# Kernel tuning notes

Hardware: AMD Instinct MI355X
Metric: run time of the kernel (lower is better)

## Reference

```python
import jax, jax.numpy as jnp
import numpy as np

B, N, DIN = 32, 4096, 256
K, D, H = 8, 256, 512
ITERS = 3
EPS = 1e-8
LN_EPS = 1e-5
SCALE = D ** -0.5


def _ln(x, g, b):
    m = jnp.mean(x, axis=-1, keepdims=True)
    v = jnp.var(x, axis=-1, keepdims=True)
    return (x - m) * jax.lax.rsqrt(v + LN_EPS) * g + b


def setup_inputs() -> dict:
    key = jax.random.key(0)
    ks = jax.random.split(key, 12)
    lin = lambda k, o, i: jax.random.uniform(k, (o, i), jnp.float32, -1.0, 1.0) * (i ** -0.5)
    return {
        "x": jax.random.normal(ks[0], (B, N, DIN), jnp.float32),
        "noise": jax.random.normal(ks[1], (B, K, D), jnp.float32),
        "nx_g": jnp.ones((DIN,), jnp.float32), "nx_b": jnp.zeros((DIN,), jnp.float32),
        "ns_g": jnp.ones((D,), jnp.float32), "ns_b": jnp.zeros((D,), jnp.float32),
        "mu": jax.random.normal(ks[2], (1, 1, D), jnp.float32) * 0.02,
        "logsigma": jnp.zeros((1, 1, D), jnp.float32),
        "Wq": lin(ks[3], D, D), "Wk": lin(ks[4], D, DIN), "Wv": lin(ks[5], D, DIN),
        "W_ih": lin(ks[6], 3 * D, D), "W_hh": lin(ks[7], 3 * D, D),
        "b_ih": jnp.zeros((3 * D,), jnp.float32), "b_hh": jnp.zeros((3 * D,), jnp.float32),
        "mlp_g": jnp.ones((D,), jnp.float32), "mlp_b": jnp.zeros((D,), jnp.float32),
        "W1": lin(ks[8], H, D), "b1": jnp.zeros((H,), jnp.float32),
        "W2": lin(ks[9], D, H), "b2": jnp.zeros((D,), jnp.float32),
    }


def _gru(u, h, W_ih, W_hh, b_ih, b_hh):
    # PyTorch GRUCell: gates ordered (r, z, n)
    gi = u @ W_ih.T + b_ih   # [BK, 3D]
    gh = h @ W_hh.T + b_hh
    ir, iz, inn = jnp.split(gi, 3, axis=-1)
    hr, hz, hn = jnp.split(gh, 3, axis=-1)
    r = jax.nn.sigmoid(ir + hr)
    z = jax.nn.sigmoid(iz + hz)
    n = jnp.tanh(inn + r * hn)
    return (1.0 - z) * n + z * h


def reference(x, noise, nx_g, nx_b, ns_g, ns_b, mu, logsigma, Wq, Wk, Wv,
              W_ih, W_hh, b_ih, b_hh, mlp_g, mlp_b, W1, b1, W2, b2):
    xn = _ln(x, nx_g, nx_b)                       # [B,N,DIN]
    k = xn @ Wk.T                                 # [B,N,D]
    v = xn @ Wv.T                                 # [B,N,D]
    slots = mu + jnp.exp(logsigma) * noise        # [B,K,D]
    attn = None
    for _ in range(ITERS):
        s = _ln(slots, ns_g, ns_b)
        q = s @ Wq.T                              # [B,K,D]
        logits = jnp.einsum('bkd,bnd->bkn', q, k) * SCALE
        attn = jax.nn.softmax(logits, axis=1) + EPS   # softmax over slots
        attn = attn / jnp.sum(attn, axis=1, keepdims=True)
        updates = jnp.einsum('bkn,bnd->bkd', attn, v)
        h = _gru(updates.reshape(B * K, D), slots.reshape(B * K, D),
                 W_ih, W_hh, b_ih, b_hh).reshape(B, K, D)
        m = _ln(h, mlp_g, mlp_b)
        m = jax.nn.gelu(m @ W1.T + b1, approximate=False) @ W2.T + b2
        slots = h + m
    return slots, attn
```

## Files before the change

### kernel.cpp

```cpp
#include <hip/hip_runtime.h>
#include <hip/hip_bf16.h>
#include <math.h>

#define LN_EPS 1e-5f
#define EPSA 1e-8f
#define SCALE 0.0625f

typedef __attribute__((ext_vector_type(8))) short short8;
typedef __attribute__((ext_vector_type(4))) short short4_t;
typedef __attribute__((ext_vector_type(4))) float f32x4;

__device__ inline unsigned short f2bf(float f) {
    union { float f; unsigned int u; } v; v.f = f;
    unsigned int r = v.u + 0x7fffu + ((v.u >> 16) & 1u);
    return (unsigned short)(r >> 16);
}
__device__ inline float bf2f(unsigned short h) {
    union { unsigned int u; float f; } v; v.u = ((unsigned int)h) << 16;
    return v.f;
}
__device__ inline float sigmoidf_(float x) { return 1.0f / (1.0f + expf(-x)); }

__global__ __launch_bounds__(256) void pack_wb(const float* __restrict__ Wk,
                                               const float* __restrict__ Wv,
                                               __hip_bfloat16* __restrict__ Wcb) {
    int idx = blockIdx.x * 256 + threadIdx.x;
    int n = idx >> 8, k = idx & 255;
    float v = (n < 256) ? Wk[n*256 + k] : Wv[(n-256)*256 + k];
    Wcb[idx] = __float2bfloat16(v);
}

__global__ __launch_bounds__(256) void gemm_kv_fused(const float* __restrict__ x,
                                                     const float* __restrict__ nx_g,
                                                     const float* __restrict__ nx_b,
                                                     const __hip_bfloat16* __restrict__ Wcb,
                                                     __hip_bfloat16* __restrict__ kp,
                                                     __hip_bfloat16* __restrict__ vp) {
    __shared__ short As[64*256];
    __shared__ float gb[512];
    const int t = threadIdx.x;
    const int row0 = blockIdx.x * 64;
    const int r = t >> 2, q = t & 3;

    float4 xr[16];
    const float* xrow = x + (size_t)(row0 + r) * 256 + q*4;
    #pragma unroll
    for (int j = 0; j < 16; ++j) xr[j] = *(const float4*)(xrow + j*16);
    gb[t] = nx_g[t]; gb[t+256] = nx_b[t];

    float s = 0.f, s2 = 0.f;
    #pragma unroll
    for (int j = 0; j < 16; ++j) {
        s  += xr[j].x + xr[j].y + xr[j].z + xr[j].w;
        s2 += xr[j].x*xr[j].x + xr[j].y*xr[j].y + xr[j].z*xr[j].z + xr[j].w*xr[j].w;
    }
    s  += __shfl_xor(s, 1);  s2 += __shfl_xor(s2, 1);
    s  += __shfl_xor(s, 2);  s2 += __shfl_xor(s2, 2);
    float m = s * (1.0f/256.0f);
    float var = s2 * (1.0f/256.0f) - m*m;
    float rstd = rsqrtf(var + LN_EPS);
    __syncthreads();

    #pragma unroll
    for (int j = 0; j < 16; ++j) {
        int c = q*4 + j*16;
        float4 g = *(const float4*)&gb[c];
        float4 bb = *(const float4*)&gb[256 + c];
        short4_t o;
        o[0] = (short)f2bf((xr[j].x - m)*rstd*g.x + bb.x);
        o[1] = (short)f2bf((xr[j].y - m)*rstd*g.y + bb.y);
        o[2] = (short)f2bf((xr[j].z - m)*rstd*g.z + bb.z);
        o[3] = (short)f2bf((xr[j].w - m)*rstd*g.w + bb.w);
        int byte = ((r << 9) + (c << 1)) ^ ((r & 7) << 4);
        *(short4_t*)((char*)As + byte) = o;
    }
    __syncthreads();

    const int l = t & 63, w = t >> 6;
    const int lr = l & 15, lk = l >> 4;
    const int arow = w*16 + lr;
    short8 af[8];
    #pragma unroll
    for (int ks = 0; ks < 8; ++ks) {
        int lin = (arow << 9) + (lk << 4) + (ks << 6);
        af[ks] = *(short8*)((char*)As + (lin ^ ((arow & 7) << 4)));
    }
    for (int c = 0; c < 8; ++c) {
        f32x4 acc[4];
        #pragma unroll
        for (int bf = 0; bf < 4; ++bf) acc[bf] = (f32x4){0.f,0.f,0.f,0.f};
        #pragma unroll
        for (int ks = 0; ks < 8; ++ks) {
            #pragma unroll
            for (int bf = 0; bf < 4; ++bf) {
                const short8 bv = *(const short8*)((const short*)Wcb +
                    ((size_t)(c*64 + bf*16 + lr))*256 + ks*32 + lk*8);
                acc[bf] = __builtin_amdgcn_mfma_f32_16x16x32_bf16(af[ks], bv, acc[bf], 0, 0, 0);
            }
        }
        __hip_bfloat16* dst = (c < 4) ? kp : vp;
        const int cb = c*64 - ((c >= 4) ? 256 : 0);
        #pragma unroll
        for (int bf = 0; bf < 4; ++bf) {
            int col = cb + bf*16 + lr;
            #pragma unroll
            for (int jj = 0; jj < 4; ++jj) {
                int row = row0 + w*16 + lk*4 + jj;
                dst[(size_t)row*256 + col] = __float2bfloat16(acc[bf][jj]);
            }
        }
    }
}

__global__ __launch_bounds__(256) void slots_init(const float* __restrict__ noise,
                                                  const float* __restrict__ mu,
                                                  const float* __restrict__ logsigma,
                                                  float* __restrict__ slots) {
    int i = blockIdx.x * 256 + threadIdx.x;
    int d = i & 255;
    slots[i] = mu[d] + expf(logsigma[d]) * noise[i];
}

__global__ __launch_bounds__(256) void qproj(const float* __restrict__ slots,
                                             const float* __restrict__ ns_g,
                                             const float* __restrict__ ns_b,
                                             const float* __restrict__ Wq,
                                             unsigned short* __restrict__ qb) {
    int row = blockIdx.x, t = threadIdx.x;
    int b = row >> 3, s8 = row & 7;
    __shared__ float sn[256];
    __shared__ float red[8];
    float v = slots[row*256 + t];
    float s = v, s2 = v*v;
    for (int off = 32; off > 0; off >>= 1) {
        s  += __shfl_down(s, off);
        s2 += __shfl_down(s2, off);
    }
    if ((t & 63) == 0) { red[t>>6] = s; red[4 + (t>>6)] = s2; }
    __syncthreads();
    float S  = red[0]+red[1]+red[2]+red[3];
    float S2 = red[4]+red[5]+red[6]+red[7];
    float m = S * (1.0f/256.0f);
    float var = S2 * (1.0f/256.0f) - m*m;
    float rs = rsqrtf(var + LN_EPS);
    sn[t] = (v - m) * rs * ns_g[t] + ns_b[t];
    __syncthreads();
    float acc = 0.0f;
    const float4* wrow = (const float4*)(Wq + t*256);
    #pragma unroll 8
    for (int i = 0; i < 64; ++i) {
        float4 w = wrow[i];
        acc += w.x*sn[4*i] + w.y*sn[4*i+1] + w.z*sn[4*i+2] + w.w*sn[4*i+3];
    }
    unsigned short hh = f2bf(acc);
    unsigned short ll = f2bf(acc - bf2f(hh));
    qb[((size_t)(b*16 + s8))*256 + t]     = hh;
    qb[((size_t)(b*16 + 8 + s8))*256 + t] = ll;
}

__global__ __launch_bounds__(256) void attn_fused(const __hip_bfloat16* __restrict__ kp,
                                                  const __hip_bfloat16* __restrict__ vp,
                                                  const unsigned short* __restrict__ qb,
                                                  float* __restrict__ attn_out,
                                                  float* __restrict__ partial) {
    __shared__ short as_[16*264];
    __shared__ float asf[8*256];
    const int b = blockIdx.x >> 4, c = blockIdx.x & 15;
    const int t = threadIdx.x, l = t & 63, w = t >> 6;
    const int lr = l & 15, lk = l >> 4;
    const int n0 = c * 256;

    short8 qf[8];
    #pragma unroll
    for (int ks = 0; ks < 8; ++ks)
        qf[ks] = *(const short8*)(qb + ((size_t)(b*16 + lr))*256 + ks*32 + lk*8);

    f32x4 acc[4];
    #pragma unroll
    for (int nf = 0; nf < 4; ++nf) acc[nf] = (f32x4){0.f,0.f,0.f,0.f};
    #pragma unroll
    for (int ks = 0; ks < 8; ++ks) {
        #pragma unroll
        for (int nf = 0; nf < 4; ++nf) {
            const short8 a = *(const short8*)((const short*)kp +
                ((size_t)(b*4096 + n0 + w*64 + nf*16 + lr))*256 + ks*32 + lk*8);
            acc[nf] = __builtin_amdgcn_mfma_f32_16x16x32_bf16(a, qf[ks], acc[nf], 0, 0, 0);
        }
    }

    const float renorm = 1.0f / (1.0f + 8.0f*EPSA);
    #pragma unroll
    for (int nf = 0; nf < 4; ++nf) {
        #pragma unroll
        for (int jj = 0; jj < 4; ++jj) {
            float lg = acc[nf][jj];
            lg += __shfl_xor(lg, 8);
            lg *= SCALE;
            float mx = lg;
            mx = fmaxf(mx, __shfl_xor(mx, 1));
            mx = fmaxf(mx, __shfl_xor(mx, 2));
            mx = fmaxf(mx, __shfl_xor(mx, 4));
            float e = expf(lg - mx);
            float ss = e;
            ss += __shfl_xor(ss, 1);
            ss += __shfl_xor(ss, 2);
            ss += __shfl_xor(ss, 4);
            acc[nf][jj] = (e / ss + EPSA) * renorm;
        }
    }

    if (lr < 8) {
        #pragma unroll
        for (int nf = 0; nf < 4; ++nf) {
            int nl = w*64 + nf*16 + lk*4;
            float4 fa = {acc[nf][0], acc[nf][1], acc[nf][2], acc[nf][3]};
            *(float4*)&asf[lr*256 + nl] = fa;
            short4_t ah, al;
            #pragma unroll
            for (int jj = 0; jj < 4; ++jj) {
                unsigned short h = f2bf(acc[nf][jj]);
                ah[jj] = (short)h;
                al[jj] = (short)f2bf(acc[nf][jj] - bf2f(h));
            }
            *(short4_t*)&as_[lr*264 + nl]       = ah;
            *(short4_t*)&as_[(8 + lr)*264 + nl] = al;
        }
    }
    __syncthreads();

    {
        int slot = t >> 5, nn = (t & 31) * 8;
        float4 f0 = *(float4*)&asf[slot*256 + nn];
        float4 f1 = *(float4*)&asf[slot*256 + nn + 4];
        float* dstp = attn_out + ((size_t)(b*8 + slot))*4096 + n0 + nn;
        *(float4*)dstp = f0;
        *(float4*)(dstp + 4) = f1;
    }

    f32x4 pacc[4];
    #pragma unroll
    for (int df = 0; df < 4; ++df) pacc[df] = (f32x4){0.f,0.f,0.f,0.f};
    #pragma unroll
    for (int ks = 0; ks < 8; ++ks) {
        const short8 a = *(const short8*)&as_[lr*264 + ks*32 + lk*8];
        #pragma unroll
        for (int df = 0; df < 4; ++df) {
            short8 bv;
            #pragma unroll
            for (int j = 0; j < 8; ++j)
                bv[j] = ((const short*)vp)[((size_t)(b*4096 + n0 + ks*32 + lk*8 + j))*256
                                           + w*64 + df*16 + lr];
            pacc[df] = __builtin_amdgcn_mfma_f32_16x16x32_bf16(a, bv, pacc[df], 0, 0, 0);
        }
    }
    #pragma unroll
    for (int df = 0; df < 4; ++df) {
        #pragma unroll
        for (int jj = 0; jj < 4; ++jj) {
            float v = pacc[df][jj];
            float vo = __shfl_xor(v, 32);
            if (l < 32) {
                int slot = lk*4 + jj;
                partial[((size_t)((b*16 + c)*8 + slot))*256 + w*64 + df*16 + lr] = v + vo;
            }
        }
    }
}

__global__ __launch_bounds__(256) void gru_mlp(const float* __restrict__ partial,
                                               const float* __restrict__ slots,
                                               const float* __restrict__ W_ih,
                                               const float* __restrict__ W_hh,
                                               const float* __restrict__ b_ih,
                                               const float* __restrict__ b_hh,
                                               const float* __restrict__ mlp_g,
                                               const float* __restrict__ mlp_b,
                                               const float* __restrict__ W1,
                                               const float* __restrict__ b1,
                                               const float* __restrict__ W2,
                                               const float* __restrict__ b2,
                                               float* __restrict__ slots_out,
                                               float* __restrict__ out_slots,
                                               int last) {
    int rrow = blockIdx.x, t = threadIdx.x;
    int b = rrow >> 3, k = rrow & 7;
    __shared__ float u_s[256], h_s[256];
    __shared__ float hn[256], m1[512];
    __shared__ float red[8];
    float u = 0.0f;
    #pragma unroll
    for (int ch = 0; ch < 16; ++ch)
        u += partial[(((size_t)(b*16 + ch)*8 + k)*256) + t];
    u_s[t] = u;
    h_s[t] = slots[rrow*256 + t];
    __syncthreads();

    float gi_r = b_ih[t], gi_z = b_ih[256 + t], gi_n = b_ih[512 + t];
    float gh_r = b_hh[t], gh_z = b_hh[256 + t], gh_n = b_hh[512 + t];
    const float4* wir = (const float4*)(W_ih + (size_t)t*256);
    const float4* wiz = (const float4*)(W_ih + (size_t)(256 + t)*256);
    const float4* win = (const float4*)(W_ih + (size_t)(512 + t)*256);
    const float4* whr = (const float4*)(W_hh + (size_t)t*256);
    const float4* whz = (const float4*)(W_hh + (size_t)(256 + t)*256);
    const float4* whn = (const float4*)(W_hh + (size_t)(512 + t)*256);
    #pragma unroll 4
    for (int i = 0; i < 64; ++i) {
        float u0 = u_s[4*i], u1 = u_s[4*i+1], u2 = u_s[4*i+2], u3 = u_s[4*i+3];
        float h0 = h_s[4*i], h1 = h_s[4*i+1], h2 = h_s[4*i+2], h3 = h_s[4*i+3];
        float4 wv;
        wv = wir[i]; gi_r += wv.x*u0 + wv.y*u1 + wv.z*u2 + wv.w*u3;
        wv = wiz[i]; gi_z += wv.x*u0 + wv.y*u1 + wv.z*u2 + wv.w*u3;
        wv = win[i]; gi_n += wv.x*u0 + wv.y*u1 + wv.z*u2 + wv.w*u3;
        wv = whr[i]; gh_r += wv.x*h0 + wv.y*h1 + wv.z*h2 + wv.w*h3;
        wv = whz[i]; gh_z += wv.x*h0 + wv.y*h1 + wv.z*h2 + wv.w*h3;
        wv = whn[i]; gh_n += wv.x*h0 + wv.y*h1 + wv.z*h2 + wv.w*h3;
    }
    float rg = sigmoidf_(gi_r + gh_r);
    float zg = sigmoidf_(gi_z + gh_z);
    float ng = tanhf(gi_n + rg * gh_n);
    float hval = (1.0f - zg)*ng + zg*h_s[t];

    float s = hval, s2 = hval*hval;
    for (int off = 32; off > 0; off >>= 1) {
        s  += __shfl_down(s, off);
        s2 += __shfl_down(s2, off);
    }
    __syncthreads();
    if ((t & 63) == 0) { red[t>>6] = s; red[4 + (t>>6)] = s2; }
    __syncthreads();
    float S  = red[0]+red[1]+red[2]+red[3];
    float S2 = red[4]+red[5]+red[6]+red[7];
    float m = S * (1.0f/256.0f);
    float var = S2 * (1.0f/256.0f) - m*m;
    float rs = rsqrtf(var + LN_EPS);
    hn[t] = (hval - m) * rs * mlp_g[t] + mlp_b[t];
    __syncthreads();

    #pragma unroll
    for (int jj = 0; jj < 2; ++jj) {
        int j = t + jj*256;
        float acc = b1[j];
        const float4* wv = (const float4*)(W1 + (size_t)j*256);
        #pragma unroll 8
        for (int i = 0; i < 64; ++i) {
            float4 ww = wv[i];
            acc += ww.x*hn[4*i] + ww.y*hn[4*i+1] + ww.z*hn[4*i+2] + ww.w*hn[4*i+3];
        }
        m1[j] = 0.5f * acc * (1.0f + erff(acc * 0.70710678118654752f));
    }
    __syncthreads();

    float acc = b2[t];
    const float4* w2 = (const float4*)(W2 + (size_t)t*512);
    #pragma unroll 8
    for (int i = 0; i < 128; ++i) {
        float4 ww = w2[i];
        acc += ww.x*m1[4*i] + ww.y*m1[4*i+1] + ww.z*m1[4*i+2] + ww.w*m1[4*i+3];
    }
    float res = hval + acc;
    slots_out[rrow*256 + t] = res;
    if (last) out_slots[rrow*256 + t] = res;
}

extern "C" void kernel_launch(void* const* d_in, const int* in_sizes, int n_in,
                              void* d_out, int out_size, void* d_ws, size_t ws_size,
                              hipStream_t stream) {
    const float* x        = (const float*)d_in[0];
    const float* noise    = (const float*)d_in[1];
    const float* nx_g     = (const float*)d_in[2];
    const float* nx_b     = (const float*)d_in[3];
    const float* ns_g     = (const float*)d_in[4];
    const float* ns_b     = (const float*)d_in[5];
    const float* mu       = (const float*)d_in[6];
    const float* logsigma = (const float*)d_in[7];
    const float* Wq       = (const float*)d_in[8];
    const float* Wk       = (const float*)d_in[9];
    const float* Wv       = (const float*)d_in[10];
    const float* W_ih     = (const float*)d_in[11];
    const float* W_hh     = (const float*)d_in[12];
    const float* b_ih     = (const float*)d_in[13];
    const float* b_hh     = (const float*)d_in[14];
    const float* mlp_g    = (const float*)d_in[15];
    const float* mlp_b    = (const float*)d_in[16];
    const float* W1       = (const float*)d_in[17];
    const float* b1       = (const float*)d_in[18];
    const float* W2       = (const float*)d_in[19];
    const float* b2       = (const float*)d_in[20];

    float* out_slots = (float*)d_out;
    float* out_attn  = (float*)d_out + 65536;

    char* ws = (char*)d_ws;
    __hip_bfloat16* Wcb = (__hip_bfloat16*)ws;
    unsigned short* qb  = (unsigned short*)(Wcb + 131072);
    __hip_bfloat16* kp  = (__hip_bfloat16*)(qb + 131072);
    __hip_bfloat16* vp  = kp + (size_t)33554432;
    float* slots  = (float*)(vp + (size_t)33554432);
    float* partial= slots + 65536;

    pack_wb<<<512, 256, 0, stream>>>(Wk, Wv, Wcb);
    gemm_kv_fused<<<2048, 256, 0, stream>>>(x, nx_g, nx_b, Wcb, kp, vp);
    slots_init<<<256, 256, 0, stream>>>(noise, mu, logsigma, slots);

    for (int it = 0; it < 3; ++it) {
        qproj<<<256, 256, 0, stream>>>(slots, ns_g, ns_b, Wq, qb);
        attn_fused<<<512, 256, 0, stream>>>(kp, vp, qb, out_attn, partial);
        gru_mlp<<<256, 256, 0, stream>>>(partial, slots, W_ih, W_hh, b_ih, b_hh,
                                         mlp_g, mlp_b, W1, b1, W2, b2,
                                         slots, out_slots, it == 2);
    }
}
```

Before: 836.1 us.

## Fold Wk and Wv into slot side, attend directly over normalized x

Drops the big K/V projection GEMM. The query is premultiplied by Wk (q·Wkᵀ applied per slot), so logits come straight from normalized x. Attention-weighted sums of normalized x are then projected by Wv inside the GRU kernel. Normalized x is stored as a split bf16 hi/lo pair, which keeps precision but doubles the logit MFMAs and the x reads per iteration. The weighted sum over x is now done with scalar FMAs rather than MFMA, which trades tensor-core work and extra per-iteration bandwidth for removing the large precompute GEMM.

```diff
diff --git a/kernel.cpp b/kernel.cpp
--- a/kernel.cpp
+++ b/kernel.cpp
@@ -7,7 +7,6 @@
 #define SCALE 0.0625f
 
 typedef __attribute__((ext_vector_type(8))) short short8;
-typedef __attribute__((ext_vector_type(4))) short short4_t;
 typedef __attribute__((ext_vector_type(4))) float f32x4;
 
 __device__ inline unsigned short f2bf(float f) {
@@ -19,96 +18,71 @@
     union { unsigned int u; float f; } v; v.u = ((unsigned int)h) << 16;
     return v.f;
 }
+__device__ inline void bf2x(unsigned int u, float& a, float& b) {
+    union { unsigned int i; float f; } lo, hi;
+    lo.i = u << 16; hi.i = u & 0xffff0000u;
+    a = lo.f; b = hi.f;
+}
 __device__ inline float sigmoidf_(float x) { return 1.0f / (1.0f + expf(-x)); }
 
-__global__ __launch_bounds__(256) void pack_wb(const float* __restrict__ Wk,
-                                               const float* __restrict__ Wv,
-                                               __hip_bfloat16* __restrict__ Wcb) {
-    int idx = blockIdx.x * 256 + threadIdx.x;
-    int n = idx >> 8, k = idx & 255;
-    float v = (n < 256) ? Wk[n*256 + k] : Wv[(n-256)*256 + k];
-    Wcb[idx] = __float2bfloat16(v);
-}
-
-__global__ __launch_bounds__(256) void gemm_kv_fused(const float* __restrict__ x,
-                                                     const float* __restrict__ nx_g,
-                                                     const float* __restrict__ nx_b,
-                                                     const __hip_bfloat16* __restrict__ Wcb,
-                                                     __hip_bfloat16* __restrict__ kp,
-                                                     __hip_bfloat16* __restrict__ vp) {
-    __shared__ short As[64*256];
+__global__ __launch_bounds__(256) void xn_pass(const float* __restrict__ x,
+                                               const float* __restrict__ nx_g,
+                                               const float* __restrict__ nx_b,
+                                               unsigned short* __restrict__ xnh,
+                                               unsigned short* __restrict__ xnl) {
     __shared__ float gb[512];
     const int t = threadIdx.x;
-    const int row0 = blockIdx.x * 64;
-    const int r = t >> 2, q = t & 3;
-
-    float4 xr[16];
-    const float* xrow = x + (size_t)(row0 + r) * 256 + q*4;
-    #pragma unroll
-    for (int j = 0; j < 16; ++j) xr[j] = *(const float4*)(xrow + j*16);
+    const int l = t & 63, w = t >> 6;
+    const int lr = l & 15, lk = l >> 4;
+    const int row = blockIdx.x * 64 + w*16 + lr;
+
+    float4 xa[8], xb[8];
+    const float* xbase = x + (size_t)row*256 + lk*8;
+    #pragma unroll
+    for (int ks = 0; ks < 8; ++ks) {
+        xa[ks] = *(const float4*)(xbase + ks*32);
+        xb[ks] = *(const float4*)(xbase + ks*32 + 4);
+    }
     gb[t] = nx_g[t]; gb[t+256] = nx_b[t];
 
     float s = 0.f, s2 = 0.f;
     #pragma unroll
-    for (int j = 0; j < 16; ++j) {
-        s  += xr[j].x + xr[j].y + xr[j].z + xr[j].w;
-        s2 += xr[j].x*xr[j].x + xr[j].y*xr[j].y + xr[j].z*xr[j].z + xr[j].w*xr[j].w;
-    }
-    s  += __shfl_xor(s, 1);  s2 += __shfl_xor(s2, 1);
-    s  += __shfl_xor(s, 2);  s2 += __shfl_xor(s2, 2);
+    for (int ks = 0; ks < 8; ++ks) {
+        s  += xa[ks].x + xa[ks].y + xa[ks].z + xa[ks].w
+            + xb[ks].x + xb[ks].y + xb[ks].z + xb[ks].w;
+        s2 += xa[ks].x*xa[ks].x + xa[ks].y*xa[ks].y + xa[ks].z*xa[ks].z + xa[ks].w*xa[ks].w
+            + xb[ks].x*xb[ks].x + xb[ks].y*xb[ks].y + xb[ks].z*xb[ks].z + xb[ks].w*xb[ks].w;
+    }
+    s  += __shfl_xor(s, 16);  s2 += __shfl_xor(s2, 16);
+    s  += __shfl_xor(s, 32);  s2 += __shfl_xor(s2, 32);
     float m = s * (1.0f/256.0f);
     float var = s2 * (1.0f/256.0f) - m*m;
     float rstd = rsqrtf(var + LN_EPS);
     __syncthreads();
 
     #pragma unroll
-    for (int j = 0; j < 16; ++j) {
-        int c = q*4 + j*16;
-        float4 g = *(const float4*)&gb[c];
-        float4 bb = *(const float4*)&gb[256 + c];
-        short4_t o;
-        o[0] = (short)f2bf((xr[j].x - m)*rstd*g.x + bb.x);
-        o[1] = (short)f2bf((xr[j].y - m)*rstd*g.y + bb.y);
-        o[2] = (short)f2bf((xr[j].z - m)*rstd*g.z + bb.z);
-        o[3] = (short)f2bf((xr[j].w - m)*rstd*g.w + bb.w);
-        int byte = ((r << 9) + (c << 1)) ^ ((r & 7) << 4);
-        *(short4_t*)((char*)As + byte) = o;
-    }
-    __syncthreads();
-
-    const int l = t & 63, w = t >> 6;
-    const int lr = l & 15, lk = l >> 4;
-    const int arow = w*16 + lr;
-    short8 af[8];
-    #pragma unroll
     for (int ks = 0; ks < 8; ++ks) {
-        int lin = (arow << 9) + (lk << 4) + (ks << 6);
-        af[ks] = *(short8*)((char*)As + (lin ^ ((arow & 7) << 4)));
-    }
-    for (int c = 0; c < 8; ++c) {
-        f32x4 acc[4];
+        int c = ks*32 + lk*8;
+        float4 g0 = *(const float4*)&gb[c],     g1 = *(const float4*)&gb[c+4];
+        float4 b0 = *(const float4*)&gb[256+c], b1 = *(const float4*)&gb[256+c+4];
+        float e[8];
+        e[0] = (xa[ks].x - m)*rstd*g0.x + b0.x;
+        e[1] = (xa[ks].y - m)*rstd*g0.y + b0.y;
+        e[2] = (xa[ks].z - m)*rstd*g0.z + b0.z;
+        e[3] = (xa[ks].w - m)*rstd*g0.w + b0.w;
+        e[4] = (xb[ks].x - m)*rstd*g1.x + b1.x;
+        e[5] = (xb[ks].y - m)*rstd*g1.y + b1.y;
+        e[6] = (xb[ks].z - m)*rstd*g1.z + b1.z;
+        e[7] = (xb[ks].w - m)*rstd*g1.w + b1.w;
+        short8 h, lo;
         #pragma unroll
-        for (int bf = 0; bf < 4; ++bf) acc[bf] = (f32x4){0.f,0.f,0.f,0.f};
-        #pragma unroll
-        for (int ks = 0; ks < 8; ++ks) {
-            #pragma unroll
-            for (int bf = 0; bf < 4; ++bf) {
-                const short8 bv = *(const short8*)((const short*)Wcb +
-                    ((size_t)(c*64 + bf*16 + lr))*256 + ks*32 + lk*8);
-                acc[bf] = __builtin_amdgcn_mfma_f32_16x16x32_bf16(af[ks], bv, acc[bf], 0, 0, 0);
-            }
-        }
-        __hip_bfloat16* dst = (c < 4) ? kp : vp;
-        const int cb = c*64 - ((c >= 4) ? 256 : 0);
-        #pragma unroll
-        for (int bf = 0; bf < 4; ++bf) {
-            int col = cb + bf*16 + lr;
-            #pragma unroll
-            for (int jj = 0; jj < 4; ++jj) {
-                int row = row0 + w*16 + lk*4 + jj;
-                dst[(size_t)row*256 + col] = __float2bfloat16(acc[bf][jj]);
-            }
-        }
+        for (int j = 0; j < 8; ++j) {
+            unsigned short hh = f2bf(e[j]);
+            h[j]  = (short)hh;
+            lo[j] = (short)f2bf(e[j] - bf2f(hh));
+        }
+        *(short8*)(xnh + (size_t)row*256 + c) = h;
+        *(short8*)(xnl + (size_t)row*256 + c) = lo;
     }
 }
 
@@ -121,14 +95,15 @@
     slots[i] = mu[d] + expf(logsigma[d]) * noise[i];
 }
 
-__global__ __launch_bounds__(256) void qproj(const float* __restrict__ slots,
-                                             const float* __restrict__ ns_g,
-                                             const float* __restrict__ ns_b,
-                                             const float* __restrict__ Wq,
-                                             unsigned short* __restrict__ qb) {
+__global__ __launch_bounds__(256) void qkproj(const float* __restrict__ slots,
+                                              const float* __restrict__ ns_g,
+                                              const float* __restrict__ ns_b,
+                                              const float* __restrict__ Wq,
+                                              const float* __restrict__ Wk,
+                                              unsigned short* __restrict__ qkb) {
     int row = blockIdx.x, t = threadIdx.x;
     int b = row >> 3, s8 = row & 7;
-    __shared__ float sn[256];
+    __shared__ float sn[256], qs[256];
     __shared__ float red[8];
     float v = slots[row*256 + t];
     float s = v, s2 = v*v;
@@ -145,25 +120,30 @@
     float rs = rsqrtf(var + LN_EPS);
     sn[t] = (v - m) * rs * ns_g[t] + ns_b[t];
     __syncthreads();
-    float acc = 0.0f;
-    const float4* wrow = (const float4*)(Wq + t*256);
+    float qacc = 0.0f;
+    const float4* wrow = (const float4*)(Wq + (size_t)t*256);
     #pragma unroll 8
     for (int i = 0; i < 64; ++i) {
         float4 w = wrow[i];
-        acc += w.x*sn[4*i] + w.y*sn[4*i+1] + w.z*sn[4*i+2] + w.w*sn[4*i+3];
-    }
+        qacc += w.x*sn[4*i] + w.y*sn[4*i+1] + w.z*sn[4*i+2] + w.w*sn[4*i+3];
+    }
+    qs[t] = qacc;
+    __syncthreads();
+    float acc = 0.0f;
+    #pragma unroll 4
+    for (int d = 0; d < 256; ++d)
+        acc += qs[d] * Wk[(size_t)d*256 + t];
     unsigned short hh = f2bf(acc);
     unsigned short ll = f2bf(acc - bf2f(hh));
-    qb[((size_t)(b*16 + s8))*256 + t]     = hh;
-    qb[((size_t)(b*16 + 8 + s8))*256 + t] = ll;
-}
-
-__global__ __launch_bounds__(256) void attn_fused(const __hip_bfloat16* __restrict__ kp,
-                                                  const __hip_bfloat16* __restrict__ vp,
-                                                  const unsigned short* __restrict__ qb,
+    qkb[((size_t)(b*16 + s8))*256 + t]     = hh;
+    qkb[((size_t)(b*16 + 8 + s8))*256 + t] = ll;
+}
+
+__global__ __launch_bounds__(256) void attn_fused(const unsigned short* __restrict__ xnh,
+                                                  const unsigned short* __restrict__ xnl,
+                                                  const unsigned short* __restrict__ qkb,
                                                   float* __restrict__ attn_out,
                                                   float* __restrict__ partial) {
-    __shared__ short as_[16*264];
     __shared__ float asf[8*256];
     const int b = blockIdx.x >> 4, c = blockIdx.x & 15;
     const int t = threadIdx.x, l = t & 63, w = t >> 6;
@@ -173,18 +153,23 @@
     short8 qf[8];
     #pragma unroll
     for (int ks = 0; ks < 8; ++ks)
-        qf[ks] = *(const short8*)(qb + ((size_t)(b*16 + lr))*256 + ks*32 + lk*8);
-
-    f32x4 acc[4];
-    #pragma unroll
-    for (int nf = 0; nf < 4; ++nf) acc[nf] = (f32x4){0.f,0.f,0.f,0.f};
+        qf[ks] = *(const short8*)(qkb + ((size_t)(b*16 + lr))*256 + ks*32 + lk*8);
+
+    f32x4 acc1[4], acc2[4];
+    #pragma unroll
+    for (int nf = 0; nf < 4; ++nf) {
+        acc1[nf] = (f32x4){0.f,0.f,0.f,0.f};
+        acc2[nf] = (f32x4){0.f,0.f,0.f,0.f};
+    }
     #pragma unroll
     for (int ks = 0; ks < 8; ++ks) {
         #pragma unroll
         for (int nf = 0; nf < 4; ++nf) {
-            const short8 a = *(const short8*)((const short*)kp +
-                ((size_t)(b*4096 + n0 + w*64 + nf*16 + lr))*256 + ks*32 + lk*8);
-            acc[nf] = __builtin_amdgcn_mfma_f32_16x16x32_bf16(a, qf[ks], acc[nf], 0, 0, 0);
+            size_t rowoff = ((size_t)(b*4096 + n0 + w*64 + nf*16 + lr))*256 + ks*32 + lk*8;
+            short8 ah = *(const short8*)(xnh + rowoff);
+            acc1[nf] = __builtin_amdgcn_mfma_f32_16x16x32_bf16(ah, qf[ks], acc1[nf], 0, 0, 0);
+            short8 al = *(const short8*)(xnl + rowoff);
+            acc2[nf] = __builtin_amdgcn_mfma_f32_16x16x32_bf16(al, qf[ks], acc2[nf], 0, 0, 0);
         }
     }
 
@@ -193,9 +178,11 @@
     for (int nf = 0; nf < 4; ++nf) {
         #pragma unroll
         for (int jj = 0; jj < 4; ++jj) {
-            float lg = acc[nf][jj];
-            lg += __shfl_xor(lg, 8);
-            lg *= SCALE;
+            float c1 = acc1[nf][jj];
+            c1 += __shfl_xor(c1, 8);
+            float c2 = acc2[nf][jj];
+            c2 += __shfl_xor(c2, 8);
+            float lg = (c1 + c2) * SCALE;
             float mx = lg;
             mx = fmaxf(mx, __shfl_xor(mx, 1));
             mx = fmaxf(mx, __shfl_xor(mx, 2));
@@ -205,7 +192,7 @@
             ss += __shfl_xor(ss, 1);
             ss += __shfl_xor(ss, 2);
             ss += __shfl_xor(ss, 4);
-            acc[nf][jj] = (e / ss + EPSA) * renorm;
+            acc1[nf][jj] = (e / ss + EPSA) * renorm;
         }
     }
 
@@ -213,17 +200,8 @@
         #pragma unroll
         for (int nf = 0; nf < 4; ++nf) {
             int nl = w*64 + nf*16 + lk*4;
-            float4 fa = {acc[nf][0], acc[nf][1], acc[nf][2], acc[nf][3]};
+            float4 fa = {acc1[nf][0], acc1[nf][1], acc1[nf][2], acc1[nf][3]};
             *(float4*)&asf[lr*256 + nl] = fa;
-            short4_t ah, al;
-            #pragma unroll
-            for (int jj = 0; jj < 4; ++jj) {
-                unsigned short h = f2bf(acc[nf][jj]);
-                ah[jj] = (short)h;
-                al[jj] = (short)f2bf(acc[nf][jj] - bf2f(h));
-            }
-            *(short4_t*)&as_[lr*264 + nl]       = ah;
-            *(short4_t*)&as_[(8 + lr)*264 + nl] = al;
         }
     }
     __syncthreads();
@@ -237,38 +215,51 @@
         *(float4*)(dstp + 4) = f1;
     }
 
-    f32x4 pacc[4];
-    #pragma unroll
-    for (int df = 0; df < 4; ++df) pacc[df] = (f32x4){0.f,0.f,0.f,0.f};
-    #pragma unroll
-    for (int ks = 0; ks < 8; ++ks) {
-        const short8 a = *(const short8*)&as_[lr*264 + ks*32 + lk*8];
+    {
+        int ig = l & 31, no = l >> 5;
+        float pa0[8] = {0,0,0,0,0,0,0,0};
+        float pa1[8] = {0,0,0,0,0,0,0,0};
+        const unsigned short* hB = xnh + ((size_t)(b*4096 + n0))*256 + ig*8;
+        const unsigned short* lB = xnl + ((size_t)(b*4096 + n0))*256 + ig*8;
+        const float* a0row = &asf[(2*w)*256];
+        const float* a1row = &asf[(2*w+1)*256];
+        for (int n = no; n < 256; n += 2) {
+            uint4 uh = *(const uint4*)(hB + (size_t)n*256);
+            uint4 ul = *(const uint4*)(lB + (size_t)n*256);
+            float fh[8], fl[8];
+            bf2x(uh.x, fh[0], fh[1]); bf2x(uh.y, fh[2], fh[3]);
+            bf2x(uh.z, fh[4], fh[5]); bf2x(uh.w, fh[6], fh[7]);
+            bf2x(ul.x, fl[0], fl[1]); bf2x(ul.y, fl[2], fl[3]);
+            bf2x(ul.z, fl[4], fl[5]); bf2x(ul.w, fl[6], fl[7]);
+            float a0 = a0row[n], a1 = a1row[n];
+            #pragma unroll
+            for (int j = 0; j < 8; ++j) {
+                float fs = fh[j] + fl[j];
+                pa0[j] += a0 * fs;
+                pa1[j] += a1 * fs;
+            }
+        }
         #pragma unroll
-        for (int df = 0; df < 4; ++df) {
-            short8 bv;
-            #pragma unroll
-            for (int j = 0; j < 8; ++j)
-                bv[j] = ((const short*)vp)[((size_t)(b*4096 + n0 + ks*32 + lk*8 + j))*256
-                                           + w*64 + df*16 + lr];
-            pacc[df] = __builtin_amdgcn_mfma_f32_16x16x32_bf16(a, bv, pacc[df], 0, 0, 0);
-        }
-    }
-    #pragma unroll
-    for (int df = 0; df < 4; ++df) {
-        #pragma unroll
-        for (int jj = 0; jj < 4; ++jj) {
-            float v = pacc[df][jj];
-            float vo = __shfl_xor(v, 32);
-            if (l < 32) {
-                int slot = lk*4 + jj;
-                partial[((size_t)((b*16 + c)*8 + slot))*256 + w*64 + df*16 + lr] = v + vo;
-            }
+        for (int j = 0; j < 8; ++j) {
+            pa0[j] += __shfl_xor(pa0[j], 32);
+            pa1[j] += __shfl_xor(pa1[j], 32);
+        }
+        if (l < 32) {
+            float* p0 = partial + (((size_t)(b*16 + c)*8 + 2*w    )*256) + ig*8;
+            float* p1 = partial + (((size_t)(b*16 + c)*8 + 2*w + 1)*256) + ig*8;
+            float4 v0 = {pa0[0], pa0[1], pa0[2], pa0[3]};
+            float4 v1 = {pa0[4], pa0[5], pa0[6], pa0[7]};
+            float4 v2 = {pa1[0], pa1[1], pa1[2], pa1[3]};
+            float4 v3 = {pa1[4], pa1[5], pa1[6], pa1[7]};
+            *(float4*)p0 = v0; *(float4*)(p0 + 4) = v1;
+            *(float4*)p1 = v2; *(float4*)(p1 + 4) = v3;
         }
     }
 }
 
 __global__ __launch_bounds__(256) void gru_mlp(const float* __restrict__ partial,
                                                const float* __restrict__ slots,
+                                               const float* __restrict__ Wv,
                                                const float* __restrict__ W_ih,
                                                const float* __restrict__ W_hh,
                                                const float* __restrict__ b_ih,
@@ -284,15 +275,27 @@
                                                int last) {
     int rrow = blockIdx.x, t = threadIdx.x;
     int b = rrow >> 3, k = rrow & 7;
-    __shared__ float u_s[256], h_s[256];
+    __shared__ float ax_s[256], u_s[256], h_s[256];
     __shared__ float hn[256], m1[512];
     __shared__ float red[8];
-    float u = 0.0f;
+    float axv = 0.0f;
     #pragma unroll
     for (int ch = 0; ch < 16; ++ch)
-        u += partial[(((size_t)(b*16 + ch)*8 + k)*256) + t];
-    u_s[t] = u;
+        axv += partial[(((size_t)(b*16 + ch)*8 + k)*256) + t];
+    ax_s[t] = axv;
     h_s[t] = slots[rrow*256 + t];
+    __syncthreads();
+
+    float uacc = 0.0f;
+    {
+        const float4* wv = (const float4*)(Wv + (size_t)t*256);
+        #pragma unroll 8
+        for (int i = 0; i < 64; ++i) {
+            float4 ww = wv[i];
+            uacc += ww.x*ax_s[4*i] + ww.y*ax_s[4*i+1] + ww.z*ax_s[4*i+2] + ww.w*ax_s[4*i+3];
+        }
+    }
+    u_s[t] = uacc;
     __syncthreads();
 
     float gi_r = b_ih[t], gi_z = b_ih[256 + t], gi_n = b_ih[512 + t];
@@ -391,21 +394,19 @@
     float* out_attn  = (float*)d_out + 65536;
 
     char* ws = (char*)d_ws;
-    __hip_bfloat16* Wcb = (__hip_bfloat16*)ws;
-    unsigned short* qb  = (unsigned short*)(Wcb + 131072);
-    __hip_bfloat16* kp  = (__hip_bfloat16*)(qb + 131072);
-    __hip_bfloat16* vp  = kp + (size_t)33554432;
-    float* slots  = (float*)(vp + (size_t)33554432);
+    unsigned short* xnh = (unsigned short*)ws;
+    unsigned short* xnl = xnh + (size_t)33554432;
+    unsigned short* qkb = xnl + (size_t)33554432;
+    float* slots  = (float*)(qkb + 131072);
     float* partial= slots + 65536;
 
-    pack_wb<<<512, 256, 0, stream>>>(Wk, Wv, Wcb);
-    gemm_kv_fused<<<2048, 256, 0, stream>>>(x, nx_g, nx_b, Wcb, kp, vp);
+    xn_pass<<<2048, 256, 0, stream>>>(x, nx_g, nx_b, xnh, xnl);
     slots_init<<<256, 256, 0, stream>>>(noise, mu, logsigma, slots);
 
     for (int it = 0; it < 3; ++it) {
-        qproj<<<256, 256, 0, stream>>>(slots, ns_g, ns_b, Wq, qb);
-        attn_fused<<<512, 256, 0, stream>>>(kp, vp, qb, out_attn, partial);
-        gru_mlp<<<256, 256, 0, stream>>>(partial, slots, W_ih, W_hh, b_ih, b_hh,
+        qkproj<<<256, 256, 0, stream>>>(slots, ns_g, ns_b, Wq, Wk, qkb);
+        attn_fused<<<512, 256, 0, stream>>>(xnh, xnl, qkb, out_attn, partial);
+        gru_mlp<<<256, 256, 0, stream>>>(partial, slots, Wv, W_ih, W_hh, b_ih, b_hh,
                                          mlp_g, mlp_b, W1, b1, W2, b2,
                                          slots, out_slots, it == 2);
     }
```

After: 900.7 us. +7.7%, slower.
